# Performance work log

Measured on AMD Instinct MI355X. Metric: run time of the kernel, lower is better.

The kernel has to match this reference:

```python
import jax, jax.numpy as jnp
import numpy as np

B, N, D = 1, 4096, 512
H, DH, M, WIN = 8, 64, 4, 512
QK_SCALE = 10.0  # qk_norm_scale


def _l2norm(t):
    # F.normalize(p=2, dim=-1) with groups=1
    n = jnp.linalg.norm(t, axis=-1, keepdims=True)
    return t / jnp.maximum(n, 1e-12)


def _rotate_half(t):
    t1, t2 = jnp.split(t, 2, axis=-1)
    return jnp.concatenate([-t2, t1], axis=-1)


def setup_inputs() -> dict:
    key = jax.random.key(0)
    ks = jax.random.split(key, 9)
    s = 0.02
    x = jax.random.normal(ks[0], (B, N, D), jnp.float32)
    Wq = jax.random.normal(ks[1], (D, H * DH), jnp.float32) * s
    Wk = jax.random.normal(ks[2], (D, H * DH), jnp.float32) * s
    Wv = jax.random.normal(ks[3], (D, H * DH), jnp.float32) * s
    Wg = jax.random.normal(ks[4], (D, H * DH), jnp.float32) * s
    bg = jnp.ones((H * DH,), jnp.float32)  # torch init: bias=1
    Wo = jax.random.normal(ks[5], (H * DH, D), jnp.float32) * s
    mem_k = jax.random.normal(ks[6], (H, M, DH), jnp.float32)
    mem_v = jax.random.normal(ks[7], (H, M, DH), jnp.float32)
    # standard rotary table, duplicated halves so rotate_half pairing matches
    half = DH // 2
    inv = 1.0 / (10000.0 ** (np.arange(half, dtype=np.float32) / half))
    f = np.outer(np.arange(N, dtype=np.float32), inv)  # [N, DH/2]
    freqs = jnp.asarray(np.concatenate([f, f], axis=-1), jnp.float32)  # [N, DH]
    return {"x": x, "Wq": Wq, "Wk": Wk, "Wv": Wv, "Wg": Wg, "bg": bg,
            "Wo": Wo, "mem_k": mem_k, "mem_v": mem_v, "freqs": freqs}


def reference(x, Wq, Wk, Wv, Wg, bg, Wo, mem_k, mem_v, freqs):
    # projections -> b h n d
    def split_heads(t):
        return t.reshape(B, N, H, DH).transpose(0, 2, 1, 3)
    q = split_heads(x @ Wq)
    k = split_heads(x @ Wk)
    v = split_heads(x @ Wv)
    # qk-norm (groups=1), scale handled via QK_SCALE later
    q = _l2norm(q)
    k = _l2norm(k)
    # rotary (l == DH so full head dim is rotated)
    cos = jnp.cos(freqs)  # [N, DH]
    sin = jnp.sin(freqs)
    q = q * cos + _rotate_half(q) * sin
    k = k * cos + _rotate_half(k) * sin
    # memory KV concat (mem_k goes through l2norm under qk_norm)
    mk = jnp.broadcast_to(_l2norm(mem_k)[None], (B, H, M, DH))
    mv = jnp.broadcast_to(mem_v[None], (B, H, M, DH))
    k = jnp.concatenate([mk, k], axis=2)  # [B,H,M+N,DH]
    v = jnp.concatenate([mv, v], axis=2)
    J = N + M
    # local window mask: queries at positions M..J-1, keys at 0..J-1
    rq = jnp.arange(M, J)
    rk = jnp.arange(J)
    dist = rq[:, None] - rk[None, :]
    allowed = (dist <= WIN) & (dist >= -WIN)  # [N, J]
    sim = jnp.einsum('bhid,bhjd->bhij', q, k) * QK_SCALE
    neg = -jnp.finfo(sim.dtype).max
    sim = jnp.where(allowed[None, None], sim, neg)
    attn = jax.nn.softmax(sim, axis=-1)
    out = jnp.einsum('bhij,bhjd->bhid', attn, v)  # [B,H,N,DH]
    out = out.transpose(0, 2, 1, 3).reshape(B, N, H * DH)
    # value gating
    gates = x @ Wg + bg
    out = out * jax.nn.sigmoid(gates)
    return out @ Wo
```

## Files before the change

kernel.cpp:

```cpp
#include <hip/hip_runtime.h>
#include <math.h>

#define TN 4096
#define DM 512
#define NH 8
#define DHD 64
#define MEM 4
#define WINR 512
#define JTOT (TN + MEM)
#define JPAD 4168
#define QK_SCALE 10.0f

typedef __attribute__((ext_vector_type(8))) short bf16x8;
typedef __attribute__((ext_vector_type(4))) float f32x4;

__device__ __forceinline__ unsigned short f2bf(float f) {
    unsigned u = __float_as_uint(f);
    u = (u + 0x7FFFu + ((u >> 16) & 1u)) >> 16;
    return (unsigned short)u;
}

__global__ __launch_bounds__(256)
void cast_x(const float* __restrict__ X, unsigned short* __restrict__ Xb)
{
    int idx = blockIdx.x * blockDim.x + threadIdx.x;
    float4 v = *(const float4*)&X[(size_t)idx * 4];
    *(ushort4*)&Xb[(size_t)idx * 4] =
        make_ushort4(f2bf(v.x), f2bf(v.y), f2bf(v.z), f2bf(v.w));
}

__global__ __launch_bounds__(256)
void transpose_cast(const float* __restrict__ W0, const float* __restrict__ W1,
                    const float* __restrict__ W2, const float* __restrict__ W3,
                    const float* __restrict__ W4, unsigned short* __restrict__ T)
{
    __shared__ unsigned short Ts[64][68];
    const int sel = blockIdx.z;
    const float* __restrict__ W =
        (sel == 0) ? W0 : (sel == 1) ? W1 : (sel == 2) ? W2 : (sel == 3) ? W3 : W4;
    unsigned short* __restrict__ Wt = T + (size_t)sel * DM * DM;
    const int r0 = blockIdx.x * 64;
    const int c0 = blockIdx.y * 64;
    const int t = threadIdx.x;

    #pragma unroll
    for (int p = 0; p < 4; ++p) {
        int i  = p * 16 + (t >> 4);
        int j4 = (t & 15) * 4;
        float4 v = *(const float4*)&W[(size_t)(r0 + i) * DM + c0 + j4];
        Ts[i][j4 + 0] = f2bf(v.x); Ts[i][j4 + 1] = f2bf(v.y);
        Ts[i][j4 + 2] = f2bf(v.z); Ts[i][j4 + 3] = f2bf(v.w);
    }
    __syncthreads();
    #pragma unroll
    for (int p = 0; p < 4; ++p) {
        int oc  = p * 16 + (t >> 4);
        int or4 = (t & 15) * 4;
        *(ushort4*)&Wt[(size_t)(c0 + oc) * DM + r0 + or4] =
            make_ushort4(Ts[or4 + 0][oc], Ts[or4 + 1][oc],
                         Ts[or4 + 2][oc], Ts[or4 + 3][oc]);
    }
}

__global__ __launch_bounds__(256)
void gemm_qkvg_mfma(const unsigned short* __restrict__ Xb,
                    const unsigned short* __restrict__ Wt,
                    float* __restrict__ q_ws, float* __restrict__ k_ws,
                    unsigned short* __restrict__ v_b, float* __restrict__ graw)
{
    __shared__ __align__(16) unsigned short As[128][32];
    __shared__ __align__(16) unsigned short Bs[128][32];
    const int sel = blockIdx.z;
    const unsigned short* __restrict__ Wsel = Wt + (size_t)sel * DM * DM;
    const int row0 = blockIdx.x * 128;
    const int col0 = blockIdx.y * 128;
    const int t = threadIdx.x;
    const int w = t >> 6, l = t & 63;
    const int wm = w >> 1, wn = w & 1;

    f32x4 acc[4][4];
    #pragma unroll
    for (int mi = 0; mi < 4; ++mi)
        #pragma unroll
        for (int ni = 0; ni < 4; ++ni)
            acc[mi][ni] = (f32x4){0.f, 0.f, 0.f, 0.f};

    for (int k0 = 0; k0 < DM; k0 += 32) {
        __syncthreads();
        #pragma unroll
        for (int cc = 0; cc < 2; ++cc) {
            int c = t + cc * 256;
            int row = c >> 2, k8 = c & 3;
            *(bf16x8*)&As[row][k8 * 8] =
                *(const bf16x8*)&Xb[(size_t)(row0 + row) * DM + k0 + k8 * 8];
            *(bf16x8*)&Bs[row][k8 * 8] =
                *(const bf16x8*)&Wsel[(size_t)(col0 + row) * DM + k0 + k8 * 8];
        }
        __syncthreads();

        bf16x8 af[4], bfr[4];
        #pragma unroll
        for (int mi = 0; mi < 4; ++mi)
            af[mi] = *(const bf16x8*)&As[wm * 64 + mi * 16 + (l & 15)][(l >> 4) * 8];
        #pragma unroll
        for (int ni = 0; ni < 4; ++ni)
            bfr[ni] = *(const bf16x8*)&Bs[wn * 64 + ni * 16 + (l & 15)][(l >> 4) * 8];
        #pragma unroll
        for (int mi = 0; mi < 4; ++mi)
            #pragma unroll
            for (int ni = 0; ni < 4; ++ni)
                acc[mi][ni] = __builtin_amdgcn_mfma_f32_16x16x32_bf16(
                    af[mi], bfr[ni], acc[mi][ni], 0, 0, 0);
    }

    #pragma unroll
    for (int mi = 0; mi < 4; ++mi) {
        #pragma unroll
        for (int ni = 0; ni < 4; ++ni) {
            int gcol = col0 + wn * 64 + ni * 16 + (l & 15);
            int h = gcol >> 6, d = gcol & 63;
            #pragma unroll
            for (int r = 0; r < 4; ++r) {
                int grow = row0 + wm * 64 + mi * 16 + (l >> 4) * 4 + r;
                float v = acc[mi][ni][r];
                if (sel == 3)      graw[(size_t)grow * DM + gcol] = v;
                else if (sel == 0) q_ws[(((size_t)h * TN + grow) << 6) + d] = v;
                else if (sel == 1) k_ws[(((size_t)h * JPAD + MEM + grow) << 6) + d] = v;
                else               v_b[((size_t)h * JPAD + MEM + grow) * 64 + d] = f2bf(v);
            }
        }
    }
}

__global__ __launch_bounds__(256)
void gemm_out_mfma(const unsigned short* __restrict__ Ab,
                   const unsigned short* __restrict__ Wot,
                   float* __restrict__ C)
{
    __shared__ __align__(16) unsigned short As[128][32];
    __shared__ __align__(16) unsigned short Bs[128][32];
    const int row0 = blockIdx.x * 128;
    const int col0 = blockIdx.y * 128;
    const int t = threadIdx.x;
    const int w = t >> 6, l = t & 63;
    const int wm = w >> 1, wn = w & 1;

    f32x4 acc[4][4];
    #pragma unroll
    for (int mi = 0; mi < 4; ++mi)
        #pragma unroll
        for (int ni = 0; ni < 4; ++ni)
            acc[mi][ni] = (f32x4){0.f, 0.f, 0.f, 0.f};

    for (int k0 = 0; k0 < DM; k0 += 32) {
        __syncthreads();
        #pragma unroll
        for (int cc = 0; cc < 2; ++cc) {
            int c = t + cc * 256;
            int row = c >> 2, k8 = c & 3;
            *(bf16x8*)&As[row][k8 * 8] =
                *(const bf16x8*)&Ab[(size_t)(row0 + row) * DM + k0 + k8 * 8];
            *(bf16x8*)&Bs[row][k8 * 8] =
                *(const bf16x8*)&Wot[(size_t)(col0 + row) * DM + k0 + k8 * 8];
        }
        __syncthreads();

        bf16x8 af[4], bfr[4];
        #pragma unroll
        for (int mi = 0; mi < 4; ++mi)
            af[mi] = *(const bf16x8*)&As[wm * 64 + mi * 16 + (l & 15)][(l >> 4) * 8];
        #pragma unroll
        for (int ni = 0; ni < 4; ++ni)
            bfr[ni] = *(const bf16x8*)&Bs[wn * 64 + ni * 16 + (l & 15)][(l >> 4) * 8];
        #pragma unroll
        for (int mi = 0; mi < 4; ++mi)
            #pragma unroll
            for (int ni = 0; ni < 4; ++ni)
                acc[mi][ni] = __builtin_amdgcn_mfma_f32_16x16x32_bf16(
                    af[mi], bfr[ni], acc[mi][ni], 0, 0, 0);
    }

    #pragma unroll
    for (int mi = 0; mi < 4; ++mi)
        #pragma unroll
        for (int ni = 0; ni < 4; ++ni) {
            int gcol = col0 + wn * 64 + ni * 16 + (l & 15);
            #pragma unroll
            for (int r = 0; r < 4; ++r) {
                int grow = row0 + wm * 64 + mi * 16 + (l >> 4) * 4 + r;
                C[(size_t)grow * DM + gcol] = acc[mi][ni][r];
            }
        }
}

__global__ __launch_bounds__(256)
void qk_norm_rope(float* __restrict__ q_ws, float* __restrict__ k_ws,
                  float* __restrict__ graw, const float* __restrict__ freqs,
                  const float* __restrict__ bg)
{
    int gw   = (blockIdx.x * blockDim.x + threadIdx.x) >> 6;
    int lane = threadIdx.x & 63;
    int h = gw >> 12;
    int n = gw & 4095;

    float* qrow = &q_ws[((size_t)h * TN + n) << 6];
    float* krow = &k_ws[((size_t)h * JPAD + MEM + n) << 6];
    float qv = qrow[lane];
    float kv = krow[lane];

    float sq = qv * qv;
    float sk = kv * kv;
    #pragma unroll
    for (int off = 1; off < 64; off <<= 1) {
        sq += __shfl_xor(sq, off);
        sk += __shfl_xor(sk, off);
    }
    qv = qv / fmaxf(sqrtf(sq), 1e-12f);
    kv = kv / fmaxf(sqrtf(sk), 1e-12f);

    float f = freqs[(size_t)n * DHD + lane];
    float sn, cs;
    sincosf(f, &sn, &cs);
    float qo = __shfl_xor(qv, 32); qo = (lane < 32) ? -qo : qo;
    float ko = __shfl_xor(kv, 32); ko = (lane < 32) ? -ko : ko;
    float qr = qv * cs + qo * sn;
    float kr = kv * cs + ko * sn;

    asm volatile("" ::: "memory");
    ((unsigned short*)qrow)[lane] = f2bf(qr);
    ((unsigned short*)krow)[lane] = f2bf(kr);

    size_t gi = (size_t)n * DM + h * DHD + lane;
    float g = graw[gi] + bg[h * DHD + lane];
    graw[gi] = 1.0f / (1.0f + __expf(-g));
}

__global__ void mem_init(const float* __restrict__ mem_k,
                         const float* __restrict__ mem_v,
                         float* __restrict__ k_ws, unsigned short* __restrict__ v_b)
{
    int gw   = (blockIdx.x * blockDim.x + threadIdx.x) >> 6;
    int lane = threadIdx.x & 63;
    if (gw >= NH * MEM) return;
    int h = gw >> 2, m = gw & 3;
    float kv = mem_k[(size_t)(h * MEM + m) * DHD + lane];
    float s = kv * kv;
    #pragma unroll
    for (int off = 1; off < 64; off <<= 1) s += __shfl_xor(s, off);
    kv = kv / fmaxf(sqrtf(s), 1e-12f);
    ((unsigned short*)k_ws)[(((size_t)h * JPAD + m) << 7) + lane] = f2bf(kv);
    v_b[((size_t)h * JPAD + m) * 64 + lane] = f2bf(mem_v[(size_t)(h * MEM + m) * DHD + lane]);
}

__global__ __launch_bounds__(256)
void attn_mfma(const unsigned short* __restrict__ qb,
               const unsigned short* __restrict__ kb,
               const unsigned short* __restrict__ vb,
               const float* __restrict__ gate,
               unsigned short* __restrict__ attnb)
{
    __shared__ __align__(16) unsigned short Qs[64][72];
    __shared__ __align__(16) unsigned short Ks[64][72];
    __shared__ __align__(16) unsigned short Vt[64][72];
    __shared__ __align__(16) unsigned short Ps[64][72];

    const int sw   = (blockIdx.x & 7) * 64 + (blockIdx.x >> 3);
    const int head = sw >> 6;
    const int n0   = (sw & 63) * 64;
    const int t = threadIdx.x;
    const int wid = t >> 6;
    const int l = t & 63;
    const int l15 = l & 15, lh = l >> 4;

    #pragma unroll
    for (int it = 0; it < 2; ++it) {
        int idx = t + it * 256;
        int row = idx >> 3, c8 = (idx & 7) * 8;
        *(bf16x8*)&Qs[row][c8] =
            *(const bf16x8*)&qb[((size_t)(head * TN + n0 + row) << 7) + c8];
    }

    f32x4 oacc[4];
    #pragma unroll
    for (int dt = 0; dt < 4; ++dt) oacc[dt] = (f32x4){0.f, 0.f, 0.f, 0.f};
    float mrow[4] = {-3.0e38f, -3.0e38f, -3.0e38f, -3.0e38f};
    float lrow[4] = {0.f, 0.f, 0.f, 0.f};

    const int p_base = MEM + n0;
    const int kstart = max(0, p_base - WINR);
    const int kend   = min(JTOT, p_base + 63 + WINR + 1);

    for (int j0 = kstart; j0 < kend; j0 += 64) {
        __syncthreads();
        #pragma unroll
        for (int it = 0; it < 2; ++it) {
            int idx = t + it * 256;
            int row = idx >> 3, c8 = (idx & 7) * 8;
            *(bf16x8*)&Ks[row][c8] =
                *(const bf16x8*)&kb[((size_t)(head * JPAD + j0 + row) << 7) + c8];
            int j = idx & 63, d0 = (idx >> 6) * 8;
            bf16x8 vv = *(const bf16x8*)&vb[(size_t)(head * JPAD + j0 + j) * 64 + d0];
            #pragma unroll
            for (int i = 0; i < 8; ++i) Vt[d0 + i][j] = (unsigned short)vv[i];
        }
        __syncthreads();

        f32x4 sacc[4];
        #pragma unroll
        for (int kt = 0; kt < 4; ++kt) sacc[kt] = (f32x4){0.f, 0.f, 0.f, 0.f};
        #pragma unroll
        for (int s = 0; s < 2; ++s) {
            bf16x8 a = *(const bf16x8*)&Qs[wid * 16 + l15][s * 32 + lh * 8];
            #pragma unroll
            for (int kt = 0; kt < 4; ++kt) {
                bf16x8 b = *(const bf16x8*)&Ks[kt * 16 + l15][s * 32 + lh * 8];
                sacc[kt] = __builtin_amdgcn_mfma_f32_16x16x32_bf16(a, b, sacc[kt], 0, 0, 0);
            }
        }

        #pragma unroll
        for (int r = 0; r < 4; ++r) {
            int pq = p_base + wid * 16 + lh * 4 + r;
            float sv[4];
            float tm = -3.0e38f;
            #pragma unroll
            for (int kt = 0; kt < 4; ++kt) {
                int j = j0 + kt * 16 + l15;
                int dist = pq - j;
                bool ok = (dist <= WINR) && (dist >= -WINR) && (j < JTOT);
                float val = ok ? sacc[kt][r] * QK_SCALE : -3.0e38f;
                sv[kt] = val;
                tm = fmaxf(tm, val);
            }
            #pragma unroll
            for (int off = 1; off < 16; off <<= 1) tm = fmaxf(tm, __shfl_xor(tm, off));
            float mnew = fmaxf(mrow[r], tm);
            float corr = __expf(mrow[r] - mnew);
            float rs = 0.f;
            #pragma unroll
            for (int kt = 0; kt < 4; ++kt) {
                float pe = (sv[kt] > -1.0e37f) ? __expf(sv[kt] - mnew) : 0.f;
                rs += pe;
                Ps[wid * 16 + lh * 4 + r][kt * 16 + l15] = f2bf(pe);
            }
            #pragma unroll
            for (int off = 1; off < 16; off <<= 1) rs += __shfl_xor(rs, off);
            lrow[r] = lrow[r] * corr + rs;
            mrow[r] = mnew;
            #pragma unroll
            for (int dt = 0; dt < 4; ++dt) oacc[dt][r] *= corr;
        }
        __syncthreads();

        #pragma unroll
        for (int s = 0; s < 2; ++s) {
            bf16x8 a = *(const bf16x8*)&Ps[wid * 16 + l15][s * 32 + lh * 8];
            #pragma unroll
            for (int dt = 0; dt < 4; ++dt) {
                bf16x8 b = *(const bf16x8*)&Vt[dt * 16 + l15][s * 32 + lh * 8];
                oacc[dt] = __builtin_amdgcn_mfma_f32_16x16x32_bf16(a, b, oacc[dt], 0, 0, 0);
            }
        }
    }

    #pragma unroll
    for (int r = 0; r < 4; ++r) {
        int n = n0 + wid * 16 + lh * 4 + r;
        float inv = 1.0f / lrow[r];
        #pragma unroll
        for (int dt = 0; dt < 4; ++dt) {
            int col = head * 64 + dt * 16 + l15;
            float g = gate[(size_t)n * DM + col];
            attnb[(size_t)n * DM + col] = f2bf(oacc[dt][r] * inv * g);
        }
    }
}

extern "C" void kernel_launch(void* const* d_in, const int* in_sizes, int n_in,
                              void* d_out, int out_size, void* d_ws, size_t ws_size,
                              hipStream_t stream)
{
    const float* x     = (const float*)d_in[0];
    const float* Wq    = (const float*)d_in[1];
    const float* Wk    = (const float*)d_in[2];
    const float* Wv    = (const float*)d_in[3];
    const float* Wg    = (const float*)d_in[4];
    const float* bg    = (const float*)d_in[5];
    const float* Wo    = (const float*)d_in[6];
    const float* mem_k = (const float*)d_in[7];
    const float* mem_v = (const float*)d_in[8];
    const float* freqs = (const float*)d_in[9];

    float* q_ws = (float*)d_ws;
    float* k_ws = q_ws + (size_t)NH * TN * DHD;
    float* graw = k_ws + (size_t)NH * JPAD * DHD;
    unsigned short* v_b   = (unsigned short*)(graw + (size_t)TN * DM);
    unsigned short* Xb    = v_b + (size_t)NH * JPAD * DHD;
    unsigned short* attnb = Xb;
    unsigned short* Wt    = Xb + (size_t)TN * DM;

    cast_x<<<dim3(TN * DM / 4 / 256), 256, 0, stream>>>(x, Xb);

    transpose_cast<<<dim3(8, 8, 5), 256, 0, stream>>>(Wq, Wk, Wv, Wg, Wo, Wt);

    gemm_qkvg_mfma<<<dim3(TN / 128, DM / 128, 4), 256, 0, stream>>>(
        Xb, Wt, q_ws, k_ws, v_b, graw);

    qk_norm_rope<<<dim3(NH * TN / 4), 256, 0, stream>>>(q_ws, k_ws, graw, freqs, bg);

    mem_init<<<dim3(8), 256, 0, stream>>>(mem_k, mem_v, k_ws, v_b);

    attn_mfma<<<dim3(512), 256, 0, stream>>>(
        (const unsigned short*)q_ws, (const unsigned short*)k_ws, v_b, graw, attnb);

    gemm_out_mfma<<<dim3(TN / 128, DM / 128), 256, 0, stream>>>(
        attnb, Wt + (size_t)4 * DM * DM, (float*)d_out);
}
```

Measured before the change: 176.8 us.

## Fuse prep kernels, fold qk-norm/rope/gate into GEMM epilogue, prefetch K/V in attention

Merges the x cast, weight transposes, sincos table and memory-KV init into one prep launch. Moves the l2-norm, rotary and sigmoid gating into the QKVG GEMM epilogue so Q/K are written directly as bf16, removing the separate norm/rope kernel and its fp32 round trip. The attention loop now register-prefetches the next K/V tile, drops one barrier per iteration and raises wave priority around the MFMA sections. In exchange the GEMM epilogue does more work and reads a precomputed cos/sin table. The removed barrier leaves Ps and Vt reuse protected only by the barrier at the top of the next iteration.

```diff
diff --git a/kernel.cpp b/kernel.cpp
--- a/kernel.cpp
+++ b/kernel.cpp
@@ -21,52 +21,81 @@
 }
 
 __global__ __launch_bounds__(256)
-void cast_x(const float* __restrict__ X, unsigned short* __restrict__ Xb)
+void prep(const float* __restrict__ X, unsigned short* __restrict__ Xb,
+          const float* __restrict__ W0, const float* __restrict__ W1,
+          const float* __restrict__ W2, const float* __restrict__ W3,
+          const float* __restrict__ W4, unsigned short* __restrict__ T,
+          const float* __restrict__ freqs, float2* __restrict__ tab,
+          const float* __restrict__ mem_k, const float* __restrict__ mem_v,
+          unsigned short* __restrict__ k_b, unsigned short* __restrict__ v_b)
 {
-    int idx = blockIdx.x * blockDim.x + threadIdx.x;
-    float4 v = *(const float4*)&X[(size_t)idx * 4];
-    *(ushort4*)&Xb[(size_t)idx * 4] =
-        make_ushort4(f2bf(v.x), f2bf(v.y), f2bf(v.z), f2bf(v.w));
-}
-
-__global__ __launch_bounds__(256)
-void transpose_cast(const float* __restrict__ W0, const float* __restrict__ W1,
-                    const float* __restrict__ W2, const float* __restrict__ W3,
-                    const float* __restrict__ W4, unsigned short* __restrict__ T)
-{
-    __shared__ unsigned short Ts[64][68];
-    const int sel = blockIdx.z;
-    const float* __restrict__ W =
-        (sel == 0) ? W0 : (sel == 1) ? W1 : (sel == 2) ? W2 : (sel == 3) ? W3 : W4;
-    unsigned short* __restrict__ Wt = T + (size_t)sel * DM * DM;
-    const int r0 = blockIdx.x * 64;
-    const int c0 = blockIdx.y * 64;
+    const int b = blockIdx.x;
     const int t = threadIdx.x;
 
-    #pragma unroll
-    for (int p = 0; p < 4; ++p) {
-        int i  = p * 16 + (t >> 4);
-        int j4 = (t & 15) * 4;
-        float4 v = *(const float4*)&W[(size_t)(r0 + i) * DM + c0 + j4];
-        Ts[i][j4 + 0] = f2bf(v.x); Ts[i][j4 + 1] = f2bf(v.y);
-        Ts[i][j4 + 2] = f2bf(v.z); Ts[i][j4 + 3] = f2bf(v.w);
-    }
-    __syncthreads();
-    #pragma unroll
-    for (int p = 0; p < 4; ++p) {
-        int oc  = p * 16 + (t >> 4);
-        int or4 = (t & 15) * 4;
-        *(ushort4*)&Wt[(size_t)(c0 + oc) * DM + r0 + or4] =
-            make_ushort4(Ts[or4 + 0][oc], Ts[or4 + 1][oc],
-                         Ts[or4 + 2][oc], Ts[or4 + 3][oc]);
+    if (b < 2048) {
+        int idx = b * 256 + t;
+        float4 v = *(const float4*)&X[(size_t)idx * 4];
+        *(ushort4*)&Xb[(size_t)idx * 4] =
+            make_ushort4(f2bf(v.x), f2bf(v.y), f2bf(v.z), f2bf(v.w));
+    } else if (b < 2368) {
+        __shared__ unsigned short Ts[64][68];
+        int bi = b - 2048;
+        int sel = bi >> 6, tile = bi & 63;
+        const float* __restrict__ W =
+            (sel == 0) ? W0 : (sel == 1) ? W1 : (sel == 2) ? W2 : (sel == 3) ? W3 : W4;
+        unsigned short* __restrict__ Wt = T + (size_t)sel * DM * DM;
+        int r0 = (tile >> 3) * 64, c0 = (tile & 7) * 64;
+        #pragma unroll
+        for (int p = 0; p < 4; ++p) {
+            int i  = p * 16 + (t >> 4);
+            int j4 = (t & 15) * 4;
+            float4 v = *(const float4*)&W[(size_t)(r0 + i) * DM + c0 + j4];
+            Ts[i][j4 + 0] = f2bf(v.x); Ts[i][j4 + 1] = f2bf(v.y);
+            Ts[i][j4 + 2] = f2bf(v.z); Ts[i][j4 + 3] = f2bf(v.w);
+        }
+        __syncthreads();
+        #pragma unroll
+        for (int p = 0; p < 4; ++p) {
+            int oc  = p * 16 + (t >> 4);
+            int or4 = (t & 15) * 4;
+            *(ushort4*)&Wt[(size_t)(c0 + oc) * DM + r0 + or4] =
+                make_ushort4(Ts[or4 + 0][oc], Ts[or4 + 1][oc],
+                             Ts[or4 + 2][oc], Ts[or4 + 3][oc]);
+        }
+    } else if (b < 2432) {
+        int tid = (b - 2368) * 256 + t;
+        #pragma unroll
+        for (int e = 0; e < 16; ++e) {
+            int id = e * 16384 + tid;
+            float f = freqs[id];
+            float sn, cs;
+            sincosf(f, &sn, &cs);
+            tab[id] = make_float2(cs, sn);
+        }
+    } else {
+        int gw   = (b - 2432) * 4 + (t >> 6);
+        int lane = t & 63;
+        int h = gw >> 2, m = gw & 3;
+        float kv = mem_k[(size_t)(h * MEM + m) * DHD + lane];
+        float s = kv * kv;
+        #pragma unroll
+        for (int off = 1; off < 64; off <<= 1) s += __shfl_xor(s, off);
+        kv = kv / fmaxf(sqrtf(s), 1e-12f);
+        k_b[((size_t)h * JPAD + m) * 64 + lane] = f2bf(kv);
+        v_b[((size_t)h * JPAD + m) * 64 + lane] =
+            f2bf(mem_v[(size_t)(h * MEM + m) * DHD + lane]);
     }
 }
 
 __global__ __launch_bounds__(256)
 void gemm_qkvg_mfma(const unsigned short* __restrict__ Xb,
                     const unsigned short* __restrict__ Wt,
-                    float* __restrict__ q_ws, float* __restrict__ k_ws,
-                    unsigned short* __restrict__ v_b, float* __restrict__ graw)
+                    const float2* __restrict__ tab,
+                    const float* __restrict__ bg,
+                    unsigned short* __restrict__ q_b,
+                    unsigned short* __restrict__ k_b,
+                    unsigned short* __restrict__ v_b,
+                    float* __restrict__ graw)
 {
     __shared__ __align__(16) unsigned short As[128][32];
     __shared__ __align__(16) unsigned short Bs[128][32];
@@ -77,6 +106,7 @@
     const int t = threadIdx.x;
     const int w = t >> 6, l = t & 63;
     const int wm = w >> 1, wn = w & 1;
+    const int l15 = l & 15, lh = l >> 4;
 
     f32x4 acc[4][4];
     #pragma unroll
@@ -101,10 +131,10 @@
         bf16x8 af[4], bfr[4];
         #pragma unroll
         for (int mi = 0; mi < 4; ++mi)
-            af[mi] = *(const bf16x8*)&As[wm * 64 + mi * 16 + (l & 15)][(l >> 4) * 8];
+            af[mi] = *(const bf16x8*)&As[wm * 64 + mi * 16 + l15][lh * 8];
         #pragma unroll
         for (int ni = 0; ni < 4; ++ni)
-            bfr[ni] = *(const bf16x8*)&Bs[wn * 64 + ni * 16 + (l & 15)][(l >> 4) * 8];
+            bfr[ni] = *(const bf16x8*)&Bs[wn * 64 + ni * 16 + l15][lh * 8];
         #pragma unroll
         for (int mi = 0; mi < 4; ++mi)
             #pragma unroll
@@ -113,22 +143,62 @@
                     af[mi], bfr[ni], acc[mi][ni], 0, 0, 0);
     }
 
-    #pragma unroll
-    for (int mi = 0; mi < 4; ++mi) {
-        #pragma unroll
-        for (int ni = 0; ni < 4; ++ni) {
-            int gcol = col0 + wn * 64 + ni * 16 + (l & 15);
-            int h = gcol >> 6, d = gcol & 63;
+    if (sel <= 1) {
+        const int h = (col0 + wn * 64) >> 6;
+        #pragma unroll
+        for (int mi = 0; mi < 4; ++mi) {
             #pragma unroll
             for (int r = 0; r < 4; ++r) {
-                int grow = row0 + wm * 64 + mi * 16 + (l >> 4) * 4 + r;
-                float v = acc[mi][ni][r];
-                if (sel == 3)      graw[(size_t)grow * DM + gcol] = v;
-                else if (sel == 0) q_ws[(((size_t)h * TN + grow) << 6) + d] = v;
-                else if (sel == 1) k_ws[(((size_t)h * JPAD + MEM + grow) << 6) + d] = v;
-                else               v_b[((size_t)h * JPAD + MEM + grow) * 64 + d] = f2bf(v);
-            }
-        }
+                float v0 = acc[mi][0][r], v1 = acc[mi][1][r];
+                float v2 = acc[mi][2][r], v3 = acc[mi][3][r];
+                float ss = v0 * v0 + v1 * v1 + v2 * v2 + v3 * v3;
+                ss += __shfl_xor(ss, 1); ss += __shfl_xor(ss, 2);
+                ss += __shfl_xor(ss, 4); ss += __shfl_xor(ss, 8);
+                float inv = 1.0f / fmaxf(sqrtf(ss), 1e-12f);
+                v0 *= inv; v1 *= inv; v2 *= inv; v3 *= inv;
+                int n = row0 + wm * 64 + mi * 16 + lh * 4 + r;
+                float2 t0 = tab[n * 64 + l15];
+                float2 t1 = tab[n * 64 + 16 + l15];
+                float o0 = v0 * t0.x - v2 * t0.y;
+                float o1 = v1 * t1.x - v3 * t1.y;
+                float o2 = v2 * t0.x + v0 * t0.y;
+                float o3 = v3 * t1.x + v1 * t1.y;
+                unsigned short* dst = (sel == 0)
+                    ? &q_b[((size_t)h * TN + n) * 64]
+                    : &k_b[((size_t)h * JPAD + MEM + n) * 64];
+                dst[l15]      = f2bf(o0);
+                dst[16 + l15] = f2bf(o1);
+                dst[32 + l15] = f2bf(o2);
+                dst[48 + l15] = f2bf(o3);
+            }
+        }
+    } else if (sel == 2) {
+        const int h = (col0 + wn * 64) >> 6;
+        #pragma unroll
+        for (int mi = 0; mi < 4; ++mi)
+            #pragma unroll
+            for (int ni = 0; ni < 4; ++ni) {
+                int d = ni * 16 + l15;
+                #pragma unroll
+                for (int r = 0; r < 4; ++r) {
+                    int grow = row0 + wm * 64 + mi * 16 + lh * 4 + r;
+                    v_b[((size_t)h * JPAD + MEM + grow) * 64 + d] = f2bf(acc[mi][ni][r]);
+                }
+            }
+    } else {
+        #pragma unroll
+        for (int mi = 0; mi < 4; ++mi)
+            #pragma unroll
+            for (int ni = 0; ni < 4; ++ni) {
+                int gcol = col0 + wn * 64 + ni * 16 + l15;
+                float bgv = bg[gcol];
+                #pragma unroll
+                for (int r = 0; r < 4; ++r) {
+                    int grow = row0 + wm * 64 + mi * 16 + lh * 4 + r;
+                    float g = acc[mi][ni][r] + bgv;
+                    graw[(size_t)grow * DM + gcol] = 1.0f / (1.0f + __expf(-g));
+                }
+            }
     }
 }
 
@@ -194,65 +264,6 @@
 }
 
 __global__ __launch_bounds__(256)
-void qk_norm_rope(float* __restrict__ q_ws, float* __restrict__ k_ws,
-                  float* __restrict__ graw, const float* __restrict__ freqs,
-                  const float* __restrict__ bg)
-{
-    int gw   = (blockIdx.x * blockDim.x + threadIdx.x) >> 6;
-    int lane = threadIdx.x & 63;
-    int h = gw >> 12;
-    int n = gw & 4095;
-
-    float* qrow = &q_ws[((size_t)h * TN + n) << 6];
-    float* krow = &k_ws[((size_t)h * JPAD + MEM + n) << 6];
-    float qv = qrow[lane];
-    float kv = krow[lane];
-
-    float sq = qv * qv;
-    float sk = kv * kv;
-    #pragma unroll
-    for (int off = 1; off < 64; off <<= 1) {
-        sq += __shfl_xor(sq, off);
-        sk += __shfl_xor(sk, off);
-    }
-    qv = qv / fmaxf(sqrtf(sq), 1e-12f);
-    kv = kv / fmaxf(sqrtf(sk), 1e-12f);
-
-    float f = freqs[(size_t)n * DHD + lane];
-    float sn, cs;
-    sincosf(f, &sn, &cs);
-    float qo = __shfl_xor(qv, 32); qo = (lane < 32) ? -qo : qo;
-    float ko = __shfl_xor(kv, 32); ko = (lane < 32) ? -ko : ko;
-    float qr = qv * cs + qo * sn;
-    float kr = kv * cs + ko * sn;
-
-    asm volatile("" ::: "memory");
-    ((unsigned short*)qrow)[lane] = f2bf(qr);
-    ((unsigned short*)krow)[lane] = f2bf(kr);
-
-    size_t gi = (size_t)n * DM + h * DHD + lane;
-    float g = graw[gi] + bg[h * DHD + lane];
-    graw[gi] = 1.0f / (1.0f + __expf(-g));
-}
-
-__global__ void mem_init(const float* __restrict__ mem_k,
-                         const float* __restrict__ mem_v,
-                         float* __restrict__ k_ws, unsigned short* __restrict__ v_b)
-{
-    int gw   = (blockIdx.x * blockDim.x + threadIdx.x) >> 6;
-    int lane = threadIdx.x & 63;
-    if (gw >= NH * MEM) return;
-    int h = gw >> 2, m = gw & 3;
-    float kv = mem_k[(size_t)(h * MEM + m) * DHD + lane];
-    float s = kv * kv;
-    #pragma unroll
-    for (int off = 1; off < 64; off <<= 1) s += __shfl_xor(s, off);
-    kv = kv / fmaxf(sqrtf(s), 1e-12f);
-    ((unsigned short*)k_ws)[(((size_t)h * JPAD + m) << 7) + lane] = f2bf(kv);
-    v_b[((size_t)h * JPAD + m) * 64 + lane] = f2bf(mem_v[(size_t)(h * MEM + m) * DHD + lane]);
-}
-
-__global__ __launch_bounds__(256)
 void attn_mfma(const unsigned short* __restrict__ qb,
                const unsigned short* __restrict__ kb,
                const unsigned short* __restrict__ vb,
@@ -277,7 +288,7 @@
         int idx = t + it * 256;
         int row = idx >> 3, c8 = (idx & 7) * 8;
         *(bf16x8*)&Qs[row][c8] =
-            *(const bf16x8*)&qb[((size_t)(head * TN + n0 + row) << 7) + c8];
+            *(const bf16x8*)&qb[((size_t)(head * TN + n0 + row)) * 64 + c8];
     }
 
     f32x4 oacc[4];
@@ -290,24 +301,39 @@
     const int kstart = max(0, p_base - WINR);
     const int kend   = min(JTOT, p_base + 63 + WINR + 1);
 
+    const int srow = t >> 3, sc8 = (t & 7) * 8;
+    const int srow2 = (t + 256) >> 3, sc82 = ((t + 256) & 7) * 8;
+    const int vj = t & 63, vd0 = (t >> 6) * 8;
+    const int vj2 = (t + 256) & 63, vd02 = ((t + 256) >> 6) * 8;
+    bf16x8 kr0, kr1, vr0, vr1;
+
+    kr0 = *(const bf16x8*)&kb[((size_t)head * JPAD + kstart + srow) * 64 + sc8];
+    kr1 = *(const bf16x8*)&kb[((size_t)head * JPAD + kstart + srow2) * 64 + sc82];
+    vr0 = *(const bf16x8*)&vb[((size_t)head * JPAD + kstart + vj) * 64 + vd0];
+    vr1 = *(const bf16x8*)&vb[((size_t)head * JPAD + kstart + vj2) * 64 + vd02];
+
     for (int j0 = kstart; j0 < kend; j0 += 64) {
         __syncthreads();
-        #pragma unroll
-        for (int it = 0; it < 2; ++it) {
-            int idx = t + it * 256;
-            int row = idx >> 3, c8 = (idx & 7) * 8;
-            *(bf16x8*)&Ks[row][c8] =
-                *(const bf16x8*)&kb[((size_t)(head * JPAD + j0 + row) << 7) + c8];
-            int j = idx & 63, d0 = (idx >> 6) * 8;
-            bf16x8 vv = *(const bf16x8*)&vb[(size_t)(head * JPAD + j0 + j) * 64 + d0];
-            #pragma unroll
-            for (int i = 0; i < 8; ++i) Vt[d0 + i][j] = (unsigned short)vv[i];
-        }
-        __syncthreads();
+        *(bf16x8*)&Ks[srow][sc8]   = kr0;
+        *(bf16x8*)&Ks[srow2][sc82] = kr1;
+        #pragma unroll
+        for (int i = 0; i < 8; ++i) Vt[vd0 + i][vj]   = (unsigned short)vr0[i];
+        #pragma unroll
+        for (int i = 0; i < 8; ++i) Vt[vd02 + i][vj2] = (unsigned short)vr1[i];
+        __syncthreads();
+
+        if (j0 + 64 < kend) {
+            int jn = j0 + 64;
+            kr0 = *(const bf16x8*)&kb[((size_t)head * JPAD + jn + srow) * 64 + sc8];
+            kr1 = *(const bf16x8*)&kb[((size_t)head * JPAD + jn + srow2) * 64 + sc82];
+            vr0 = *(const bf16x8*)&vb[((size_t)head * JPAD + jn + vj) * 64 + vd0];
+            vr1 = *(const bf16x8*)&vb[((size_t)head * JPAD + jn + vj2) * 64 + vd02];
+        }
 
         f32x4 sacc[4];
         #pragma unroll
         for (int kt = 0; kt < 4; ++kt) sacc[kt] = (f32x4){0.f, 0.f, 0.f, 0.f};
+        __builtin_amdgcn_s_setprio(1);
         #pragma unroll
         for (int s = 0; s < 2; ++s) {
             bf16x8 a = *(const bf16x8*)&Qs[wid * 16 + l15][s * 32 + lh * 8];
@@ -317,6 +343,7 @@
                 sacc[kt] = __builtin_amdgcn_mfma_f32_16x16x32_bf16(a, b, sacc[kt], 0, 0, 0);
             }
         }
+        __builtin_amdgcn_s_setprio(0);
 
         #pragma unroll
         for (int r = 0; r < 4; ++r) {
@@ -350,8 +377,8 @@
             #pragma unroll
             for (int dt = 0; dt < 4; ++dt) oacc[dt][r] *= corr;
         }
-        __syncthreads();
-
+
+        __builtin_amdgcn_s_setprio(1);
         #pragma unroll
         for (int s = 0; s < 2; ++s) {
             bf16x8 a = *(const bf16x8*)&Ps[wid * 16 + l15][s * 32 + lh * 8];
@@ -361,6 +388,7 @@
                 oacc[dt] = __builtin_amdgcn_mfma_f32_16x16x32_bf16(a, b, oacc[dt], 0, 0, 0);
             }
         }
+        __builtin_amdgcn_s_setprio(0);
     }
 
     #pragma unroll
@@ -391,27 +419,22 @@
     const float* mem_v = (const float*)d_in[8];
     const float* freqs = (const float*)d_in[9];
 
-    float* q_ws = (float*)d_ws;
-    float* k_ws = q_ws + (size_t)NH * TN * DHD;
-    float* graw = k_ws + (size_t)NH * JPAD * DHD;
-    unsigned short* v_b   = (unsigned short*)(graw + (size_t)TN * DM);
-    unsigned short* Xb    = v_b + (size_t)NH * JPAD * DHD;
+    unsigned short* q_b = (unsigned short*)d_ws;
+    unsigned short* k_b = q_b + (size_t)NH * TN * DHD;
+    unsigned short* v_b = k_b + (size_t)NH * JPAD * DHD;
+    unsigned short* Xb  = v_b + (size_t)NH * JPAD * DHD;
     unsigned short* attnb = Xb;
-    unsigned short* Wt    = Xb + (size_t)TN * DM;
-
-    cast_x<<<dim3(TN * DM / 4 / 256), 256, 0, stream>>>(x, Xb);
-
-    transpose_cast<<<dim3(8, 8, 5), 256, 0, stream>>>(Wq, Wk, Wv, Wg, Wo, Wt);
+    unsigned short* Wt  = Xb + (size_t)TN * DM;
+    float* graw = (float*)(Wt + (size_t)5 * DM * DM);
+    float2* tab = (float2*)(graw + (size_t)TN * DM);
+
+    prep<<<dim3(2440), 256, 0, stream>>>(x, Xb, Wq, Wk, Wv, Wg, Wo, Wt,
+                                         freqs, tab, mem_k, mem_v, k_b, v_b);
 
     gemm_qkvg_mfma<<<dim3(TN / 128, DM / 128, 4), 256, 0, stream>>>(
-        Xb, Wt, q_ws, k_ws, v_b, graw);
-
-    qk_norm_rope<<<dim3(NH * TN / 4), 256, 0, stream>>>(q_ws, k_ws, graw, freqs, bg);
-
-    mem_init<<<dim3(8), 256, 0, stream>>>(mem_k, mem_v, k_ws, v_b);
-
-    attn_mfma<<<dim3(512), 256, 0, stream>>>(
-        (const unsigned short*)q_ws, (const unsigned short*)k_ws, v_b, graw, attnb);
+        Xb, Wt, tab, bg, q_b, k_b, v_b, graw);
+
+    attn_mfma<<<dim3(512), 256, 0, stream>>>(q_b, k_b, v_b, graw, attnb);
 
     gemm_out_mfma<<<dim3(TN / 128, DM / 128), 256, 0, stream>>>(
         attnb, Wt + (size_t)4 * DM * DM, (float*)d_out);
```

Measured after the change: 173.6 us. No clear change (-1.8%).
